# Optimization experiments

Measured on AMD Instinct MI355X. Metric: run time of the kernel, lower is better.

Reference implementation:

```python
import jax, jax.numpy as jnp
import numpy as np

N_WIRES = 25                    # odd -> RX on wire 0, then SingleExcitation on (1,2),(3,4),...,(23,24)
DIM = 2 ** N_WIRES              # 33_554_432 amplitudes
N_THETA = (N_WIRES + 1) // 2    # 13


def _apply_rx(state, th, wire):
    """Apply RX(th) = [[cos, -i sin], [-i sin, cos]] (half-angle) to `wire`.
    PennyLane convention: wire 0 is the most-significant bit of the amplitude index."""
    c = jnp.cos(th * 0.5)
    ms = -1j * jnp.sin(th * 0.5)
    st = state.reshape(2 ** wire, 2, -1)          # [pre, 2, post]
    s0, s1 = st[:, 0], st[:, 1]
    new = jnp.stack([c * s0 + ms * s1, ms * s0 + c * s1], axis=1)
    return new.reshape(-1)


def _apply_single_excitation(state, phi, wire):
    """SingleExcitation(phi) on wires [wire, wire+1]: rotates the |01>,|10> subspace
    by angle phi/2; |00>,|11> untouched."""
    c = jnp.cos(phi * 0.5)
    s = jnp.sin(phi * 0.5)
    st = state.reshape(2 ** wire, 2, 2, -1)       # [pre, q_i, q_{i+1}, post]
    a00, a01, a10, a11 = st[:, 0, 0], st[:, 0, 1], st[:, 1, 0], st[:, 1, 1]
    n01 = c * a01 - s * a10
    n10 = s * a01 + c * a10
    new = jnp.stack([jnp.stack([a00, n01], axis=1),
                     jnp.stack([n10, a11], axis=1)], axis=1)
    return new.reshape(-1)


def setup_inputs() -> dict:
    key = jax.random.key(0)
    kf, kt = jax.random.split(key)
    feature = jax.random.normal(kf, (DIM,), dtype=jnp.float32)
    # he_normal init on shape (13, 1): std = sqrt(2 / fan_in) with fan_in = 13
    theta = jax.random.normal(kt, (N_THETA, 1), dtype=jnp.float32) * np.sqrt(2.0 / N_THETA)
    return {"feature": feature, "theta": theta}


def reference(feature, theta) -> jnp.ndarray:
    # AmplitudeEmbedding with pad_with=0.0: pad (no-op here, len == 2^n) then L2-normalize
    state = (feature / jnp.linalg.norm(feature)).astype(jnp.complex64)
    # odd wire count: RX(theta[0][0]) on wire 0, start pair gates at wire 1
    state = _apply_rx(state, theta[0, 0], 0)
    for i in range(1, N_WIRES, 2):                # i = 1,3,...,23 -> theta[0..11]
        state = _apply_single_excitation(state, theta[i // 2, 0], i)
    return jnp.real(state)
```

## Files before the change

### kernel.cpp

```cpp
#include <hip/hip_runtime.h>
#include <math.h>


typedef float f32x4 __attribute__((ext_vector_type(4)));

static __device__ __forceinline__ float4 nt_load4(const float* p) {
    f32x4 v = __builtin_nontemporal_load((const f32x4*)p);
    return *(float4*)&v;
}
static __device__ __forceinline__ void nt_store4(float* p, float4 v) {
    __builtin_nontemporal_store(*(f32x4*)&v, (f32x4*)p);
}

static __device__ __forceinline__ void bar_lgkm() {
    asm volatile("s_waitcnt lgkmcnt(0)\n\ts_barrier" ::: "memory");
}

static __device__ __forceinline__ void rot4(float4& a, float4& b, float c, float s) {
    float4 na, nb;
    na.x = c*a.x - s*b.x;  nb.x = s*a.x + c*b.x;
    na.y = c*a.y - s*b.y;  nb.y = s*a.y + c*b.y;
    na.z = c*a.z - s*b.z;  nb.z = s*a.z + c*b.z;
    na.w = c*a.w - s*b.w;  nb.w = s*a.w + c*b.w;
    a = na; b = nb;
}

static __device__ __forceinline__ float4 shflx4(float4 v, int m) {
    float4 r;
    r.x = __shfl_xor(v.x, m, 64);
    r.y = __shfl_xor(v.y, m, 64);
    r.z = __shfl_xor(v.z, m, 64);
    r.w = __shfl_xor(v.w, m, 64);
    return r;
}

template <int NR>
static __device__ __forceinline__ void rotshfl(float4* f, int sh, float c, float s, int lane) {
    const int pv = (lane >> sh) & 3;
    const bool act = (pv == 1) || (pv == 2);
    const float cl = act ? c : 1.0f;
    const float sl = act ? ((pv == 1) ? -s : s) : 0.0f;
    const int m = 3 << sh;
#pragma unroll
    for (int k = 0; k < NR; ++k) {
        float4 p = shflx4(f[k], m);
        float4 n;
        n.x = fmaf(sl, p.x, cl * f[k].x);
        n.y = fmaf(sl, p.y, cl * f[k].y);
        n.z = fmaf(sl, p.z, cl * f[k].z);
        n.w = fmaf(sl, p.w, cl * f[k].w);
        f[k] = n;
    }
}

__global__ __launch_bounds__(256, 2) void qnn_p1(const float* __restrict__ in,
                                                 const float* __restrict__ theta,
                                                 float* __restrict__ out,
                                                 double* __restrict__ partials) {
    __shared__ __align__(16) float4 lds[4096];
    __shared__ double red[4];
    const int t = threadIdx.x, lane = t & 63, w2 = t >> 6;
    const long gA = (long)blockIdx.x << 13;
    const long gB = gA + 4096;

    float c0,s0,c1,s1,c2,s2,c3,s3,c4,s4,c5,s5,c6,s6;
    { float th;
      th=0.5f*theta[11]; c0=cosf(th); s0=sinf(th);
      th=0.5f*theta[10]; c1=cosf(th); s1=sinf(th);
      th=0.5f*theta[9];  c2=cosf(th); s2=sinf(th);
      th=0.5f*theta[8];  c3=cosf(th); s3=sinf(th);
      th=0.5f*theta[7];  c4=cosf(th); s4=sinf(th);
      th=0.5f*theta[6];  c5=cosf(th); s5=sinf(th);
      th=0.5f*theta[5];  c6=cosf(th); s6=sinf(th); }

    float4 f[16], g[16];
#pragma unroll
    for (int k = 0; k < 16; ++k)
        f[k] = nt_load4(in + ((gA + ((w2 << 10) | (k << 6) | lane)) << 2));
#pragma unroll
    for (int k = 0; k < 16; ++k)
        g[k] = nt_load4(in + ((gB + ((w2 << 10) | (k << 6) | lane)) << 2));

    double acc = 0.0;
#pragma unroll
    for (int k = 0; k < 16; ++k)
        acc += (double)f[k].x*f[k].x + (double)f[k].y*f[k].y
             + (double)f[k].z*f[k].z + (double)f[k].w*f[k].w;

#pragma unroll
    for (int k = 0; k < 16; ++k) {
        float ny = c0*f[k].y - s0*f[k].z;
        float nz = s0*f[k].y + c0*f[k].z;
        f[k].y = ny; f[k].z = nz;
    }
    rotshfl<16>(f, 0, c1, s1, lane);
    rotshfl<16>(f, 2, c2, s2, lane);
    rotshfl<16>(f, 4, c3, s3, lane);
#pragma unroll
    for (int hi = 0; hi < 16; hi += 4) rot4(f[hi+1], f[hi+2], c4, s4);
#pragma unroll
    for (int lo = 0; lo < 4; ++lo)     rot4(f[4+lo], f[8+lo], c5, s5);

#pragma unroll
    for (int k = 0; k < 16; ++k) lds[(w2 << 10) | (k << 6) | lane] = f[k];
    bar_lgkm();
#pragma unroll
    for (int m = 0; m < 16; ++m) f[m] = lds[(m << 8) | (w2 << 6) | lane];
#pragma unroll
    for (int lo = 0; lo < 4; ++lo) rot4(f[4+lo], f[8+lo], c6, s6);
#pragma unroll
    for (int m = 0; m < 16; ++m)
        *(float4*)(out + ((gA + ((m << 8) | (w2 << 6) | lane)) << 2)) = f[m];

#pragma unroll
    for (int k = 0; k < 16; ++k)
        acc += (double)g[k].x*g[k].x + (double)g[k].y*g[k].y
             + (double)g[k].z*g[k].z + (double)g[k].w*g[k].w;
#pragma unroll
    for (int k = 0; k < 16; ++k) {
        float ny = c0*g[k].y - s0*g[k].z;
        float nz = s0*g[k].y + c0*g[k].z;
        g[k].y = ny; g[k].z = nz;
    }
    rotshfl<16>(g, 0, c1, s1, lane);
    rotshfl<16>(g, 2, c2, s2, lane);
    rotshfl<16>(g, 4, c3, s3, lane);
#pragma unroll
    for (int hi = 0; hi < 16; hi += 4) rot4(g[hi+1], g[hi+2], c4, s4);
#pragma unroll
    for (int lo = 0; lo < 4; ++lo)     rot4(g[4+lo], g[8+lo], c5, s5);

    bar_lgkm();
#pragma unroll
    for (int k = 0; k < 16; ++k) lds[(w2 << 10) | (k << 6) | lane] = g[k];
    bar_lgkm();
#pragma unroll
    for (int m = 0; m < 16; ++m) g[m] = lds[(m << 8) | (w2 << 6) | lane];
#pragma unroll
    for (int lo = 0; lo < 4; ++lo) rot4(g[4+lo], g[8+lo], c6, s6);
#pragma unroll
    for (int m = 0; m < 16; ++m)
        *(float4*)(out + ((gB + ((m << 8) | (w2 << 6) | lane)) << 2)) = g[m];

#pragma unroll
    for (int off = 32; off > 0; off >>= 1) acc += __shfl_down(acc, off, 64);
    if (lane == 0) red[w2] = acc;
    bar_lgkm();
    if (t == 0)
        partials[blockIdx.x] = red[0] + red[1] + red[2] + red[3];
}

__global__ void qnn_norm(const double* __restrict__ partials,
                         const float* __restrict__ theta,
                         double* __restrict__ scale) {
    __shared__ double w[4];
    const int t = threadIdx.x;
    double acc = 0.0;
    for (int i = t; i < 1024; i += 256) acc += partials[i];
#pragma unroll
    for (int off = 32; off > 0; off >>= 1) acc += __shfl_down(acc, off, 64);
    if ((t & 63) == 0) w[t >> 6] = acc;
    __syncthreads();
    if (t == 0) {
        double tot = w[0] + w[1] + w[2] + w[3];
        *scale = (double)cosf(0.5f * theta[0]) / sqrt(tot);
    }
}

__global__ __launch_bounds__(512, 2) void qnn_high(float* __restrict__ buf,
                                                   const float* __restrict__ theta,
                                                   const double* __restrict__ scale) {
    __shared__ __align__(16) float4 lds[8192];
    const int t = threadIdx.x, lane = t & 63, w3 = t >> 6;
    const int mid = blockIdx.x;
    const long gqA = (long)mid << 3;
    const long gqB = (1L << 22) | ((long)mid << 3);

    float c7,s7,c8,s8,c9,s9,c10,s10,c11,s11;
    { float th;
      th=0.5f*theta[4]; c7 =cosf(th); s7 =sinf(th);
      th=0.5f*theta[3]; c8 =cosf(th); s8 =sinf(th);
      th=0.5f*theta[2]; c9 =cosf(th); s9 =sinf(th);
      th=0.5f*theta[1]; c10=cosf(th); s10=sinf(th);
      th=0.5f*theta[0]; c11=cosf(th); s11=sinf(th); }
    const float sc = (float)(*scale);

    const int rbase = (w3 << 10) | ((lane >> 5) << 9) | (lane & 31);

    float4 f[16], g[16];
#pragma unroll
    for (int k = 0; k < 16; ++k) {
        const int s_ = (k << 9) | t;
        f[k] = *(const float4*)(buf + ((gqA | ((long)(s_ >> 3) << 12) | (s_ & 7)) << 2));
    }
#pragma unroll
    for (int k = 0; k < 16; ++k) {
        const int s_ = (k << 9) | t;
        g[k] = *(const float4*)(buf + ((gqB | ((long)(s_ >> 3) << 12) | (s_ & 7)) << 2));
    }

    rotshfl<16>(f, 3, c7, s7, lane);
#pragma unroll
    for (int hi = 0; hi < 16; hi += 4) rot4(f[hi+1], f[hi+2], c10, s10);
#pragma unroll
    for (int lo = 0; lo < 4; ++lo)     rot4(f[4+lo], f[8+lo], c11, s11);
#pragma unroll
    for (int k = 0; k < 16; ++k) lds[(k << 9) | t] = f[k];
    bar_lgkm();
#pragma unroll
    for (int m = 0; m < 16; ++m) f[m] = lds[rbase | (m << 5)];
#pragma unroll
    for (int hi = 0; hi < 16; hi += 4) rot4(f[hi+1], f[hi+2], c8, s8);
#pragma unroll
    for (int lo = 0; lo < 4; ++lo)     rot4(f[4+lo], f[8+lo], c9, s9);
#pragma unroll
    for (int m = 0; m < 16; ++m) {
        const int s_ = rbase | (m << 5);
        float4 v = f[m];
        v.x *= sc; v.y *= sc; v.z *= sc; v.w *= sc;
        nt_store4(buf + ((gqA | ((long)(s_ >> 3) << 12) | (s_ & 7)) << 2), v);
    }

    rotshfl<16>(g, 3, c7, s7, lane);
#pragma unroll
    for (int hi = 0; hi < 16; hi += 4) rot4(g[hi+1], g[hi+2], c10, s10);
#pragma unroll
    for (int lo = 0; lo < 4; ++lo)     rot4(g[4+lo], g[8+lo], c11, s11);
    bar_lgkm();
#pragma unroll
    for (int k = 0; k < 16; ++k) lds[(k << 9) | t] = g[k];
    bar_lgkm();
#pragma unroll
    for (int m = 0; m < 16; ++m) g[m] = lds[rbase | (m << 5)];
#pragma unroll
    for (int hi = 0; hi < 16; hi += 4) rot4(g[hi+1], g[hi+2], c8, s8);
#pragma unroll
    for (int lo = 0; lo < 4; ++lo)     rot4(g[4+lo], g[8+lo], c9, s9);
#pragma unroll
    for (int m = 0; m < 16; ++m) {
        const int s_ = rbase | (m << 5);
        float4 v = g[m];
        v.x *= sc; v.y *= sc; v.z *= sc; v.w *= sc;
        nt_store4(buf + ((gqB | ((long)(s_ >> 3) << 12) | (s_ & 7)) << 2), v);
    }
}

extern "C" void kernel_launch(void* const* d_in, const int* in_sizes, int n_in,
                              void* d_out, int out_size, void* d_ws, size_t ws_size,
                              hipStream_t stream) {
    const float* in = (const float*)d_in[0];
    const float* theta = (const float*)d_in[1];
    float* out = (float*)d_out;
    double* part = (double*)d_ws;
    double* scale = part + 1024;

    qnn_p1<<<1024, 256, 0, stream>>>(in, theta, out, part);
    qnn_norm<<<1, 256, 0, stream>>>(part, theta, scale);
    qnn_high<<<512, 512, 0, stream>>>(out, theta, scale);
}
```

Measured before the change: 97.96 us.

## Process one 4096-float4 tile per block with halved LDS and higher occupancy

The first pass now has each block handle a single 16-float4-per-thread tile instead of two, so 2048 blocks are launched and qnn_norm sums 2048 partials. The LDS transpose is cut to 2048 float4 and done in two halves, with the last rotation applied to the reordered registers and the stores issued through a permutation table. Together with launch bounds raised to 4 blocks per SM, this is meant to lower register and LDS pressure and increase occupancy for the memory-bound pass. In exchange it loses the overlap from loading the second tile early and adds barriers.

```diff
diff --git a/kernel.cpp b/kernel.cpp
--- a/kernel.cpp
+++ b/kernel.cpp
@@ -53,15 +53,14 @@
     }
 }
 
-__global__ __launch_bounds__(256, 2) void qnn_p1(const float* __restrict__ in,
+__global__ __launch_bounds__(256, 4) void qnn_p1(const float* __restrict__ in,
                                                  const float* __restrict__ theta,
                                                  float* __restrict__ out,
                                                  double* __restrict__ partials) {
-    __shared__ __align__(16) float4 lds[4096];
+    __shared__ __align__(16) float4 lds[2048];
     __shared__ double red[4];
     const int t = threadIdx.x, lane = t & 63, w2 = t >> 6;
-    const long gA = (long)blockIdx.x << 13;
-    const long gB = gA + 4096;
+    const long gfb = (long)blockIdx.x << 12;
 
     float c0,s0,c1,s1,c2,s2,c3,s3,c4,s4,c5,s5,c6,s6;
     { float th;
@@ -73,13 +72,10 @@
       th=0.5f*theta[6];  c5=cosf(th); s5=sinf(th);
       th=0.5f*theta[5];  c6=cosf(th); s6=sinf(th); }
 
-    float4 f[16], g[16];
+    float4 f[16];
 #pragma unroll
     for (int k = 0; k < 16; ++k)
-        f[k] = nt_load4(in + ((gA + ((w2 << 10) | (k << 6) | lane)) << 2));
-#pragma unroll
-    for (int k = 0; k < 16; ++k)
-        g[k] = nt_load4(in + ((gB + ((w2 << 10) | (k << 6) | lane)) << 2));
+        f[k] = nt_load4(in + ((gfb + ((w2 << 10) | (k << 6) | lane)) << 2));
 
     double acc = 0.0;
 #pragma unroll
@@ -101,46 +97,44 @@
 #pragma unroll
     for (int lo = 0; lo < 4; ++lo)     rot4(f[4+lo], f[8+lo], c5, s5);
 
-#pragma unroll
-    for (int k = 0; k < 16; ++k) lds[(w2 << 10) | (k << 6) | lane] = f[k];
-    bar_lgkm();
-#pragma unroll
-    for (int m = 0; m < 16; ++m) f[m] = lds[(m << 8) | (w2 << 6) | lane];
-#pragma unroll
-    for (int lo = 0; lo < 4; ++lo) rot4(f[4+lo], f[8+lo], c6, s6);
-#pragma unroll
-    for (int m = 0; m < 16; ++m)
-        *(float4*)(out + ((gA + ((m << 8) | (w2 << 6) | lane)) << 2)) = f[m];
-
-#pragma unroll
-    for (int k = 0; k < 16; ++k)
-        acc += (double)g[k].x*g[k].x + (double)g[k].y*g[k].y
-             + (double)g[k].z*g[k].z + (double)g[k].w*g[k].w;
-#pragma unroll
-    for (int k = 0; k < 16; ++k) {
-        float ny = c0*g[k].y - s0*g[k].z;
-        float nz = s0*g[k].y + c0*g[k].z;
-        g[k].y = ny; g[k].z = nz;
-    }
-    rotshfl<16>(g, 0, c1, s1, lane);
-    rotshfl<16>(g, 2, c2, s2, lane);
-    rotshfl<16>(g, 4, c3, s3, lane);
-#pragma unroll
-    for (int hi = 0; hi < 16; hi += 4) rot4(g[hi+1], g[hi+2], c4, s4);
-#pragma unroll
-    for (int lo = 0; lo < 4; ++lo)     rot4(g[4+lo], g[8+lo], c5, s5);
-
-    bar_lgkm();
-#pragma unroll
-    for (int k = 0; k < 16; ++k) lds[(w2 << 10) | (k << 6) | lane] = g[k];
-    bar_lgkm();
-#pragma unroll
-    for (int m = 0; m < 16; ++m) g[m] = lds[(m << 8) | (w2 << 6) | lane];
-#pragma unroll
-    for (int lo = 0; lo < 4; ++lo) rot4(g[4+lo], g[8+lo], c6, s6);
-#pragma unroll
-    for (int m = 0; m < 16; ++m)
-        *(float4*)(out + ((gB + ((m << 8) | (w2 << 6) | lane)) << 2)) = g[m];
+    const int rb = (w2 << 6) | lane;
+#pragma unroll
+    for (int k = 0; k < 8; ++k)
+        lds[(w2 << 9) | (k << 6) | lane] = f[k];
+    bar_lgkm();
+    f[0] = lds[rb];
+    f[1] = lds[(1 << 8) | rb];
+    f[2] = lds[(1 << 9) | rb];
+    f[3] = lds[(1 << 9) | (1 << 8) | rb];
+    f[4] = lds[(2 << 9) | rb];
+    f[5] = lds[(2 << 9) | (1 << 8) | rb];
+    f[6] = lds[(3 << 9) | rb];
+    f[7] = lds[(3 << 9) | (1 << 8) | rb];
+    bar_lgkm();
+#pragma unroll
+    for (int k = 8; k < 16; ++k)
+        lds[(w2 << 9) | ((k - 8) << 6) | lane] = f[k];
+    bar_lgkm();
+    f[8]  = lds[rb];
+    f[9]  = lds[(1 << 8) | rb];
+    f[10] = lds[(1 << 9) | rb];
+    f[11] = lds[(1 << 9) | (1 << 8) | rb];
+    f[12] = lds[(2 << 9) | rb];
+    f[13] = lds[(2 << 9) | (1 << 8) | rb];
+    f[14] = lds[(3 << 9) | rb];
+    f[15] = lds[(3 << 9) | (1 << 8) | rb];
+
+    rot4(f[2],  f[4],  c6, s6);
+    rot4(f[3],  f[5],  c6, s6);
+    rot4(f[10], f[12], c6, s6);
+    rot4(f[11], f[13], c6, s6);
+
+    {
+        const int M[16] = {0,1,4,5,8,9,12,13, 2,3,6,7,10,11,14,15};
+#pragma unroll
+        for (int i = 0; i < 16; ++i)
+            *(float4*)(out + ((gfb + ((M[i] << 8) | rb)) << 2)) = f[i];
+    }
 
 #pragma unroll
     for (int off = 32; off > 0; off >>= 1) acc += __shfl_down(acc, off, 64);
@@ -156,7 +150,7 @@
     __shared__ double w[4];
     const int t = threadIdx.x;
     double acc = 0.0;
-    for (int i = t; i < 1024; i += 256) acc += partials[i];
+    for (int i = t; i < 2048; i += 256) acc += partials[i];
 #pragma unroll
     for (int off = 32; off > 0; off >>= 1) acc += __shfl_down(acc, off, 64);
     if ((t & 63) == 0) w[t >> 6] = acc;
@@ -252,9 +246,9 @@
     const float* theta = (const float*)d_in[1];
     float* out = (float*)d_out;
     double* part = (double*)d_ws;
-    double* scale = part + 1024;
-
-    qnn_p1<<<1024, 256, 0, stream>>>(in, theta, out, part);
+    double* scale = part + 2048;
+
+    qnn_p1<<<2048, 256, 0, stream>>>(in, theta, out, part);
     qnn_norm<<<1, 256, 0, stream>>>(part, theta, scale);
     qnn_high<<<512, 512, 0, stream>>>(out, theta, scale);
 }
```

New measurement: 129.9 us. 32.6% more time.
